# Optimization experiments

Hardware: AMD Instinct MI355X
Metric: run time of the kernel (lower is better)

The kernel has to match this reference:

```python
import jax, jax.numpy as jnp
import numpy as np

B, L_TEXT, N_TOKEN = 8, 2048, 2048
C_TEXT, C_OUT = 3584, 384
C_HID = C_OUT * 2
CHAIN_TYPES = (1, 2)   # heavy, light
CDR_TYPES = (2, 4, 6)  # CDR1/2/3


def setup_inputs() -> dict:
    key = jax.random.key(0)
    ks = jax.random.split(key, 10)
    text_conditioning = jax.random.normal(ks[0], (B, L_TEXT, C_TEXT), jnp.float32)
    text_mask = jnp.ones((B, L_TEXT), jnp.int32)
    chain_type_ids = jax.random.randint(ks[1], (B, L_TEXT), 0, 3).astype(jnp.int32)
    cdr_region_type_ids = jax.random.randint(ks[2], (B, L_TEXT), 0, 10).astype(jnp.int32)
    boltz_chain_type = jax.random.randint(ks[3], (B, N_TOKEN), 0, 4).astype(jnp.int32)
    boltz_region_type = jax.random.randint(ks[4], (B, N_TOKEN), 0, 10).astype(jnp.int32)
    W1 = jax.random.normal(ks[5], (C_HID, C_TEXT), jnp.float32) * 0.02
    b1 = jnp.zeros((C_HID,), jnp.float32)
    W2 = jax.random.normal(ks[6], (C_OUT, C_HID), jnp.float32) * 0.02
    b2 = jnp.zeros((C_OUT,), jnp.float32)
    scale = jnp.ones((1,), jnp.float32)
    return {
        "text_conditioning": text_conditioning, "text_mask": text_mask,
        "chain_type_ids": chain_type_ids, "cdr_region_type_ids": cdr_region_type_ids,
        "boltz_chain_type": boltz_chain_type, "boltz_region_type": boltz_region_type,
        "W1": W1, "b1": b1, "W2": W2, "b2": b2, "scale": scale,
    }


def _align_one(text_proj, tmask, pmask):
    # text_proj: [L, C]; tmask: [L] bool (text CDR positions); pmask: [N] bool (protein CDR positions)
    # The k-th masked text token (in sequence order) maps to the k-th masked protein token,
    # for k < min(n_text, n_protein). Other protein positions get zeros.
    L = tmask.shape[0]
    trank = jnp.cumsum(tmask) - 1          # rank among text CDR tokens
    n_text = jnp.sum(tmask)
    prank = jnp.cumsum(pmask) - 1          # rank among protein CDR tokens
    # idx_by_rank[r] = text index whose rank is r; out-of-range scatter indices dropped
    idx_by_rank = jnp.zeros((L,), jnp.int32).at[jnp.where(tmask, trank, L)].set(
        jnp.arange(L, dtype=jnp.int32), mode="drop")
    valid = pmask & (prank < n_text)       # prank < n_protein holds by construction under pmask
    src = idx_by_rank[jnp.clip(prank, 0, L - 1)]
    emb = text_proj[src]                   # [N, C]
    return jnp.where(valid[:, None], emb, jnp.zeros((), text_proj.dtype))


def reference(text_conditioning, text_mask, chain_type_ids, cdr_region_type_ids,
              boltz_chain_type, boltz_region_type, W1, b1, W2, b2, scale):
    # 2-layer MLP projection: c_text -> 2*c_out -> c_out with SiLU
    h = jax.nn.silu(jnp.einsum("blt,ht->blh", text_conditioning, W1) + b1)
    text_proj = jnp.einsum("blh,ch->blc", h, W2) + b2    # [B, L, C_OUT]

    tm = text_mask.astype(bool)
    result = jnp.zeros((text_conditioning.shape[0], boltz_chain_type.shape[1], W2.shape[0]),
                       text_proj.dtype)
    align = jax.vmap(_align_one)
    for ct in CHAIN_TYPES:
        for rt in CDR_TYPES:
            tmask = (chain_type_ids == ct) & (cdr_region_type_ids == rt) & tm
            pmask = (boltz_chain_type == ct) & (boltz_region_type == rt)
            # (chain, cdr) pairs write to disjoint protein positions, so add is exact
            result = result + align(text_proj, tmask, pmask)
    return scale * result
```

## Files before the change

kernel.cpp:

```cpp
#include <hip/hip_runtime.h>
#include <hip/hip_bf16.h>
#include <math.h>

typedef __bf16 bf16_t;
typedef bf16_t bf16x8 __attribute__((ext_vector_type(8)));
typedef bf16_t bf16x4 __attribute__((ext_vector_type(4)));
typedef float f32x4 __attribute__((ext_vector_type(4)));

#define L_TEXT 2048
#define N_TOKEN 2048
#define C_TEXT 3584
#define C_OUT 384
#define C_HID 768
#define BATCH 8
#define MAXROWS (BATCH * N_TOKEN)
#define PM 3072
#define KSPLIT 4
#define KCHUNK (C_TEXT / KSPLIT)
#define KSPLIT2 2
#define KCHUNK2 (C_HID / KSPLIT2)

__global__ __launch_bounds__(256) void cvt_kernel(const float* __restrict__ in,
                                                  bf16_t* __restrict__ out, int n) {
    int i = (blockIdx.x * 256 + threadIdx.x) * 8;
    if (i >= n) return;
    float4 v0 = *(const float4*)(in + i);
    float4 v1 = *(const float4*)(in + i + 4);
    bf16x8 o;
    o[0] = (bf16_t)v0.x; o[1] = (bf16_t)v0.y; o[2] = (bf16_t)v0.z; o[3] = (bf16_t)v0.w;
    o[4] = (bf16_t)v1.x; o[5] = (bf16_t)v1.y; o[6] = (bf16_t)v1.z; o[7] = (bf16_t)v1.w;
    *(bf16x8*)(out + i) = o;
}

__global__ void map_kernel(const int* __restrict__ tm, const int* __restrict__ ctid,
                           const int* __restrict__ cdrid, const int* __restrict__ bct,
                           const int* __restrict__ brt,
                           int* __restrict__ rows_src, int* __restrict__ inv,
                           int* __restrict__ count) {
    __shared__ int trow[L_TEXT];
    const int bp = blockIdx.x;
    const int b = bp / 6, p = bp % 6;
    const int ct = (p < 3) ? 1 : 2;
    const int rt = 2 + 2 * (p % 3);
    const int lane = threadIdx.x;
    const unsigned long long ltm = (1ull << lane) - 1ull;

    int base = 0;
    for (int l0 = 0; l0 < L_TEXT; l0 += 64) {
        int l = l0 + lane;
        bool m = (ctid[b * L_TEXT + l] == ct) && (cdrid[b * L_TEXT + l] == rt) &&
                 (tm[b * L_TEXT + l] != 0);
        unsigned long long bal = __ballot(m);
        if (m) trow[base + __popcll(bal & ltm)] = l;
        base += __popcll(bal);
    }
    const int n_text = base;
    __syncthreads();

    base = 0;
    for (int n0 = 0; n0 < N_TOKEN; n0 += 64) {
        int n = n0 + lane;
        bool pm = (bct[b * N_TOKEN + n] == ct) && (brt[b * N_TOKEN + n] == rt);
        unsigned long long bal = __ballot(pm);
        if (pm) {
            int pr = base + __popcll(bal & ltm);
            if (pr < n_text) {
                int i = atomicAdd(count, 1);
                if (i < PM) {
                    rows_src[i] = b * L_TEXT + trow[pr];
                    inv[b * N_TOKEN + n] = i;
                }
            }
        }
        base += __popcll(bal);
    }
}

__global__ __launch_bounds__(256) void gemm1_kernel(
    const float* __restrict__ X, const bf16_t* __restrict__ W1b,
    const int* __restrict__ rows_src, const int* __restrict__ countp,
    float* __restrict__ P) {
    const int count = *countp;
    const int m0 = blockIdx.x * 64;
    if (m0 >= count) return;
    const int n0 = blockIdx.y * 128;
    const int kbeg = blockIdx.z * KCHUNK;

    __shared__ __align__(16) bf16_t As[2][64][40];
    __shared__ __align__(16) bf16_t Bs[2][128][40];

    const int t = threadIdx.x;
    const int lane = t & 63;
    const int w = t >> 6;
    const int wr = w >> 1, wc = w & 1;
    const int fr = lane & 15;
    const int kq = (lane >> 4) * 8;

    f32x4 acc[2][4];
#pragma unroll
    for (int i = 0; i < 2; i++)
#pragma unroll
        for (int j = 0; j < 4; j++) acc[i][j] = (f32x4){0.f, 0.f, 0.f, 0.f};

    const int arow = t >> 2, ac8 = (t & 3) * 8;
    const bool av = (m0 + arow < count);
    const float* ap = X + (size_t)(av ? rows_src[m0 + arow] : 0) * C_TEXT + kbeg + ac8;
    const int aofs = arow * 40 + ac8;
    const bf16_t* bp[2];
    int bofs[2];
#pragma unroll
    for (int j = 0; j < 2; j++) {
        int c = t + 256 * j;
        int row = c >> 2, c8 = (c & 3) * 8;
        bp[j] = W1b + (size_t)(n0 + row) * C_TEXT + kbeg + c8;
        bofs[j] = row * 40 + c8;
    }

    bf16_t* AsF = &As[0][0][0];
    bf16_t* BsF = &Bs[0][0][0];
    const int ABUF = 64 * 40, BBUF = 128 * 40;

    bf16x8 ra, rb0, rb1;
    {
        float4 v0 = *(const float4*)(ap);
        float4 v1 = *(const float4*)(ap + 4);
        ra[0] = (bf16_t)v0.x; ra[1] = (bf16_t)v0.y; ra[2] = (bf16_t)v0.z; ra[3] = (bf16_t)v0.w;
        ra[4] = (bf16_t)v1.x; ra[5] = (bf16_t)v1.y; ra[6] = (bf16_t)v1.z; ra[7] = (bf16_t)v1.w;
        if (!av) { for (int e = 0; e < 8; e++) ra[e] = (bf16_t)0.0f; }
        rb0 = *(const bf16x8*)(bp[0]);
        rb1 = *(const bf16x8*)(bp[1]);
    }

    const int T = KCHUNK / 32;
    for (int tile = 0; tile < T; ++tile) {
        const int cur = tile & 1;
        *(bf16x8*)(AsF + cur * ABUF + aofs) = ra;
        *(bf16x8*)(BsF + cur * BBUF + bofs[0]) = rb0;
        *(bf16x8*)(BsF + cur * BBUF + bofs[1]) = rb1;
        if (tile + 1 < T) {
            int k = (tile + 1) * 32;
            float4 v0 = *(const float4*)(ap + k);
            float4 v1 = *(const float4*)(ap + k + 4);
            bf16x8 na;
            na[0] = (bf16_t)v0.x; na[1] = (bf16_t)v0.y; na[2] = (bf16_t)v0.z; na[3] = (bf16_t)v0.w;
            na[4] = (bf16_t)v1.x; na[5] = (bf16_t)v1.y; na[6] = (bf16_t)v1.z; na[7] = (bf16_t)v1.w;
            if (!av) { for (int e = 0; e < 8; e++) na[e] = (bf16_t)0.0f; }
            bf16x8 nb0 = *(const bf16x8*)(bp[0] + k);
            bf16x8 nb1 = *(const bf16x8*)(bp[1] + k);
            __syncthreads();
            bf16x8 af[2], bfr[4];
#pragma unroll
            for (int mi = 0; mi < 2; mi++)
                af[mi] = *(const bf16x8*)(AsF + cur * ABUF + (wr * 32 + mi * 16 + fr) * 40 + kq);
#pragma unroll
            for (int ni = 0; ni < 4; ni++)
                bfr[ni] = *(const bf16x8*)(BsF + cur * BBUF + (wc * 64 + ni * 16 + fr) * 40 + kq);
#pragma unroll
            for (int mi = 0; mi < 2; mi++)
#pragma unroll
                for (int ni = 0; ni < 4; ni++)
                    acc[mi][ni] = __builtin_amdgcn_mfma_f32_16x16x32_bf16(
                        af[mi], bfr[ni], acc[mi][ni], 0, 0, 0);
            ra = na; rb0 = nb0; rb1 = nb1;
        } else {
            __syncthreads();
            bf16x8 af[2], bfr[4];
#pragma unroll
            for (int mi = 0; mi < 2; mi++)
                af[mi] = *(const bf16x8*)(AsF + cur * ABUF + (wr * 32 + mi * 16 + fr) * 40 + kq);
#pragma unroll
            for (int ni = 0; ni < 4; ni++)
                bfr[ni] = *(const bf16x8*)(BsF + cur * BBUF + (wc * 64 + ni * 16 + fr) * 40 + kq);
#pragma unroll
            for (int mi = 0; mi < 2; mi++)
#pragma unroll
                for (int ni = 0; ni < 4; ni++)
                    acc[mi][ni] = __builtin_amdgcn_mfma_f32_16x16x32_bf16(
                        af[mi], bfr[ni], acc[mi][ni], 0, 0, 0);
        }
    }

    float* Pk = P + (size_t)blockIdx.z * PM * C_HID;
    const int rj = (lane >> 4) * 4;
#pragma unroll
    for (int mi = 0; mi < 2; mi++) {
#pragma unroll
        for (int ni = 0; ni < 4; ni++) {
            int gn = n0 + wc * 64 + ni * 16 + fr;
#pragma unroll
            for (int j = 0; j < 4; j++) {
                int gm = m0 + wr * 32 + mi * 16 + rj + j;
                if (gm < count) Pk[(size_t)gm * C_HID + gn] = acc[mi][ni][j];
            }
        }
    }
}

__global__ __launch_bounds__(256) void reduce1_kernel(
    const float* __restrict__ P, const float* __restrict__ b1,
    const int* __restrict__ countp, bf16_t* __restrict__ H) {
    const int count = *countp;
    int idx = blockIdx.x * 256 + threadIdx.x;
    int m = idx / (C_HID / 4);
    int c = (idx % (C_HID / 4)) * 4;
    if (m >= count) return;
    f32x4 s = *(const f32x4*)(P + (size_t)m * C_HID + c);
#pragma unroll
    for (int ks = 1; ks < KSPLIT; ks++)
        s += *(const f32x4*)(P + ((size_t)ks * PM + m) * C_HID + c);
    f32x4 bb = *(const f32x4*)(b1 + c);
    bf16x4 o;
#pragma unroll
    for (int j = 0; j < 4; j++) {
        float v = s[j] + bb[j];
        o[j] = (bf16_t)(v / (1.0f + __expf(-v)));
    }
    *(bf16x4*)(H + (size_t)m * C_HID + c) = o;
}

__global__ __launch_bounds__(256) void gemm2_kernel(
    const bf16_t* __restrict__ Hm, const bf16_t* __restrict__ W2b,
    const int* __restrict__ countp, float* __restrict__ P2) {
    const int count = *countp;
    const int m0 = blockIdx.x * 64;
    if (m0 >= count) return;
    const int n0 = blockIdx.y * 128;
    const int kbeg = blockIdx.z * KCHUNK2;

    __shared__ __align__(16) bf16_t As[2][64][40];
    __shared__ __align__(16) bf16_t Bs[2][128][40];

    const int t = threadIdx.x;
    const int lane = t & 63;
    const int w = t >> 6;
    const int wr = w >> 1, wc = w & 1;
    const int fr = lane & 15;
    const int kq = (lane >> 4) * 8;

    f32x4 acc[2][4];
#pragma unroll
    for (int i = 0; i < 2; i++)
#pragma unroll
        for (int j = 0; j < 4; j++) acc[i][j] = (f32x4){0.f, 0.f, 0.f, 0.f};

    const int arow = t >> 2, ac8 = (t & 3) * 8;
    const bf16_t* ap = Hm + (size_t)(m0 + arow) * C_HID + kbeg + ac8;
    const int aofs = arow * 40 + ac8;
    const bf16_t* bp[2];
    int bofs[2];
#pragma unroll
    for (int j = 0; j < 2; j++) {
        int c = t + 256 * j;
        int row = c >> 2, c8 = (c & 3) * 8;
        bp[j] = W2b + (size_t)(n0 + row) * C_HID + kbeg + c8;
        bofs[j] = row * 40 + c8;
    }

    bf16_t* AsF = &As[0][0][0];
    bf16_t* BsF = &Bs[0][0][0];
    const int ABUF = 64 * 40, BBUF = 128 * 40;

    bf16x8 ra = *(const bf16x8*)(ap);
    bf16x8 rb0 = *(const bf16x8*)(bp[0]);
    bf16x8 rb1 = *(const bf16x8*)(bp[1]);

    const int T = KCHUNK2 / 32;
    for (int tile = 0; tile < T; ++tile) {
        const int cur = tile & 1;
        *(bf16x8*)(AsF + cur * ABUF + aofs) = ra;
        *(bf16x8*)(BsF + cur * BBUF + bofs[0]) = rb0;
        *(bf16x8*)(BsF + cur * BBUF + bofs[1]) = rb1;
        bf16x8 na, nb0, nb1;
        bool more = (tile + 1 < T);
        if (more) {
            int k = (tile + 1) * 32;
            na = *(const bf16x8*)(ap + k);
            nb0 = *(const bf16x8*)(bp[0] + k);
            nb1 = *(const bf16x8*)(bp[1] + k);
        }
        __syncthreads();
        bf16x8 af[2], bfr[4];
#pragma unroll
        for (int mi = 0; mi < 2; mi++)
            af[mi] = *(const bf16x8*)(AsF + cur * ABUF + (wr * 32 + mi * 16 + fr) * 40 + kq);
#pragma unroll
        for (int ni = 0; ni < 4; ni++)
            bfr[ni] = *(const bf16x8*)(BsF + cur * BBUF + (wc * 64 + ni * 16 + fr) * 40 + kq);
#pragma unroll
        for (int mi = 0; mi < 2; mi++)
#pragma unroll
            for (int ni = 0; ni < 4; ni++)
                acc[mi][ni] = __builtin_amdgcn_mfma_f32_16x16x32_bf16(
                    af[mi], bfr[ni], acc[mi][ni], 0, 0, 0);
        if (more) { ra = na; rb0 = nb0; rb1 = nb1; }
    }

    float* Pk = P2 + (size_t)blockIdx.z * PM * C_OUT;
    const int rj = (lane >> 4) * 4;
#pragma unroll
    for (int mi = 0; mi < 2; mi++) {
#pragma unroll
        for (int ni = 0; ni < 4; ni++) {
            int gn = n0 + wc * 64 + ni * 16 + fr;
#pragma unroll
            for (int j = 0; j < 4; j++) {
                int gm = m0 + wr * 32 + mi * 16 + rj + j;
                if (gm < count) Pk[(size_t)gm * C_OUT + gn] = acc[mi][ni][j];
            }
        }
    }
}

__global__ __launch_bounds__(256) void out_kernel(
    const float* __restrict__ P2, const float* __restrict__ b2,
    const int* __restrict__ inv, const float* __restrict__ scale,
    float* __restrict__ out) {
    int idx = blockIdx.x * 256 + threadIdx.x;
    int token = idx / (C_OUT / 4);
    int c = (idx % (C_OUT / 4)) * 4;
    int m = inv[token];
    f32x4 o = (f32x4){0.f, 0.f, 0.f, 0.f};
    if (m >= 0) {
        f32x4 s = *(const f32x4*)(P2 + (size_t)m * C_OUT + c);
#pragma unroll
        for (int ks = 1; ks < KSPLIT2; ks++)
            s += *(const f32x4*)(P2 + ((size_t)ks * PM + m) * C_OUT + c);
        f32x4 bb = *(const f32x4*)(b2 + c);
        const float sc = scale[0];
#pragma unroll
        for (int j = 0; j < 4; j++) o[j] = sc * (s[j] + bb[j]);
    }
    *(f32x4*)(out + (size_t)token * C_OUT + c) = o;
}

extern "C" void kernel_launch(void* const* d_in, const int* in_sizes, int n_in,
                              void* d_out, int out_size, void* d_ws, size_t ws_size,
                              hipStream_t stream) {
    const float* X     = (const float*)d_in[0];
    const int*   tm    = (const int*)d_in[1];
    const int*   ctid  = (const int*)d_in[2];
    const int*   cdrid = (const int*)d_in[3];
    const int*   bct   = (const int*)d_in[4];
    const int*   brt   = (const int*)d_in[5];
    const float* W1    = (const float*)d_in[6];
    const float* b1    = (const float*)d_in[7];
    const float* W2    = (const float*)d_in[8];
    const float* b2    = (const float*)d_in[9];
    const float* scale = (const float*)d_in[10];

    char* ws = (char*)d_ws;
    size_t off = 0;
    int* count = (int*)(ws + off);        off += 1024;
    int* rows_src = (int*)(ws + off);     off += (size_t)PM * 4;
    int* inv = (int*)(ws + off);          off += (size_t)MAXROWS * 4;
    bf16_t* W1b = (bf16_t*)(ws + off);    off += (size_t)C_HID * C_TEXT * 2;
    bf16_t* W2b = (bf16_t*)(ws + off);    off += (size_t)C_OUT * C_HID * 2;
    bf16_t* H = (bf16_t*)(ws + off);      off += (size_t)PM * C_HID * 2;
    float* P = (float*)(ws + off);        off += (size_t)KSPLIT * PM * C_HID * 4;
    float* P2 = P;

    hipMemsetAsync(count, 0, 4, stream);
    hipMemsetAsync(inv, 0xFF, (size_t)MAXROWS * 4, stream);

    cvt_kernel<<<(C_HID * C_TEXT) / 2048, 256, 0, stream>>>(W1, W1b, C_HID * C_TEXT);
    cvt_kernel<<<(C_OUT * C_HID) / 2048, 256, 0, stream>>>(W2, W2b, C_OUT * C_HID);

    map_kernel<<<BATCH * 6, 64, 0, stream>>>(tm, ctid, cdrid, bct, brt,
                                             rows_src, inv, count);

    dim3 g1(PM / 64, C_HID / 128, KSPLIT);
    gemm1_kernel<<<g1, 256, 0, stream>>>(X, W1b, rows_src, count, P);

    reduce1_kernel<<<(PM * C_HID / 4) / 256, 256, 0, stream>>>(P, b1, count, H);

    dim3 g2(PM / 64, C_OUT / 128, KSPLIT2);
    gemm2_kernel<<<g2, 256, 0, stream>>>(H, W2b, count, P2);

    out_kernel<<<(MAXROWS * C_OUT / 4) / 256, 256, 0, stream>>>(
        P2, b2, inv, scale, (float*)d_out);
}
```

Baseline: 140.8 us.

## Fuse weight conversion and workspace init into one kernel; batch map_kernel loads

Two memsets and two bf16 conversion launches are merged into one kernel that converts W1 and W2, fills the inverse index with -1 and zeroes the counter. The map kernel now loads all mask inputs up front into per-lane bitmasks with unrolled loops, then runs the ballot/compaction passes from registers, so the global loads are no longer serialized with the ballots. This targets launch overhead and memory latency in the small setup stages at the cost of somewhat more register use.

```diff
diff --git a/kernel.cpp b/kernel.cpp
--- a/kernel.cpp
+++ b/kernel.cpp
@@ -20,23 +20,47 @@
 #define KSPLIT2 2
 #define KCHUNK2 (C_HID / KSPLIT2)
 
-__global__ __launch_bounds__(256) void cvt_kernel(const float* __restrict__ in,
-                                                  bf16_t* __restrict__ out, int n) {
-    int i = (blockIdx.x * 256 + threadIdx.x) * 8;
-    if (i >= n) return;
-    float4 v0 = *(const float4*)(in + i);
-    float4 v1 = *(const float4*)(in + i + 4);
-    bf16x8 o;
-    o[0] = (bf16_t)v0.x; o[1] = (bf16_t)v0.y; o[2] = (bf16_t)v0.z; o[3] = (bf16_t)v0.w;
-    o[4] = (bf16_t)v1.x; o[5] = (bf16_t)v1.y; o[6] = (bf16_t)v1.z; o[7] = (bf16_t)v1.w;
-    *(bf16x8*)(out + i) = o;
-}
-
-__global__ void map_kernel(const int* __restrict__ tm, const int* __restrict__ ctid,
-                           const int* __restrict__ cdrid, const int* __restrict__ bct,
-                           const int* __restrict__ brt,
-                           int* __restrict__ rows_src, int* __restrict__ inv,
-                           int* __restrict__ count) {
+#define NW1 (C_HID * C_TEXT / 8)
+#define NW2 (C_OUT * C_HID / 8)
+#define NINV (MAXROWS / 4)
+#define NINIT (NW1 + NW2 + NINV + 1)
+
+__global__ __launch_bounds__(256) void init_cvt_kernel(
+    const float* __restrict__ W1, const float* __restrict__ W2,
+    bf16_t* __restrict__ W1b, bf16_t* __restrict__ W2b,
+    int* __restrict__ inv, int* __restrict__ count) {
+    int idx = blockIdx.x * 256 + threadIdx.x;
+    if (idx < NW1) {
+        int i = idx * 8;
+        float4 v0 = *(const float4*)(W1 + i);
+        float4 v1 = *(const float4*)(W1 + i + 4);
+        bf16x8 o;
+        o[0] = (bf16_t)v0.x; o[1] = (bf16_t)v0.y; o[2] = (bf16_t)v0.z; o[3] = (bf16_t)v0.w;
+        o[4] = (bf16_t)v1.x; o[5] = (bf16_t)v1.y; o[6] = (bf16_t)v1.z; o[7] = (bf16_t)v1.w;
+        *(bf16x8*)(W1b + i) = o;
+    } else if (idx < NW1 + NW2) {
+        int i = (idx - NW1) * 8;
+        float4 v0 = *(const float4*)(W2 + i);
+        float4 v1 = *(const float4*)(W2 + i + 4);
+        bf16x8 o;
+        o[0] = (bf16_t)v0.x; o[1] = (bf16_t)v0.y; o[2] = (bf16_t)v0.z; o[3] = (bf16_t)v0.w;
+        o[4] = (bf16_t)v1.x; o[5] = (bf16_t)v1.y; o[6] = (bf16_t)v1.z; o[7] = (bf16_t)v1.w;
+        *(bf16x8*)(W2b + i) = o;
+    } else if (idx < NW1 + NW2 + NINV) {
+        int i = idx - NW1 - NW2;
+        int4 m1 = {-1, -1, -1, -1};
+        ((int4*)inv)[i] = m1;
+    } else if (idx == NW1 + NW2 + NINV) {
+        *count = 0;
+    }
+}
+
+__global__ __launch_bounds__(64) void map_kernel(
+    const int* __restrict__ tm, const int* __restrict__ ctid,
+    const int* __restrict__ cdrid, const int* __restrict__ bct,
+    const int* __restrict__ brt,
+    int* __restrict__ rows_src, int* __restrict__ inv,
+    int* __restrict__ count) {
     __shared__ int trow[L_TEXT];
     const int bp = blockIdx.x;
     const int b = bp / 6, p = bp % 6;
@@ -45,30 +69,46 @@
     const int lane = threadIdx.x;
     const unsigned long long ltm = (1ull << lane) - 1ull;
 
+    unsigned int tbits = 0, pbits = 0;
+#pragma unroll
+    for (int i = 0; i < 32; i++) {
+        int l = i * 64 + lane;
+        unsigned int m = (ctid[b * L_TEXT + l] == ct) &&
+                         (cdrid[b * L_TEXT + l] == rt) &&
+                         (tm[b * L_TEXT + l] != 0);
+        tbits |= m << i;
+    }
+#pragma unroll
+    for (int i = 0; i < 32; i++) {
+        int n = i * 64 + lane;
+        unsigned int m = (bct[b * N_TOKEN + n] == ct) &&
+                         (brt[b * N_TOKEN + n] == rt);
+        pbits |= m << i;
+    }
+
     int base = 0;
-    for (int l0 = 0; l0 < L_TEXT; l0 += 64) {
-        int l = l0 + lane;
-        bool m = (ctid[b * L_TEXT + l] == ct) && (cdrid[b * L_TEXT + l] == rt) &&
-                 (tm[b * L_TEXT + l] != 0);
+#pragma unroll
+    for (int i = 0; i < 32; i++) {
+        bool m = (tbits >> i) & 1;
         unsigned long long bal = __ballot(m);
-        if (m) trow[base + __popcll(bal & ltm)] = l;
+        if (m) trow[base + __popcll(bal & ltm)] = i * 64 + lane;
         base += __popcll(bal);
     }
     const int n_text = base;
     __syncthreads();
 
     base = 0;
-    for (int n0 = 0; n0 < N_TOKEN; n0 += 64) {
-        int n = n0 + lane;
-        bool pm = (bct[b * N_TOKEN + n] == ct) && (brt[b * N_TOKEN + n] == rt);
-        unsigned long long bal = __ballot(pm);
-        if (pm) {
+#pragma unroll
+    for (int i = 0; i < 32; i++) {
+        bool m = (pbits >> i) & 1;
+        unsigned long long bal = __ballot(m);
+        if (m) {
             int pr = base + __popcll(bal & ltm);
             if (pr < n_text) {
-                int i = atomicAdd(count, 1);
-                if (i < PM) {
-                    rows_src[i] = b * L_TEXT + trow[pr];
-                    inv[b * N_TOKEN + n] = i;
+                int idx = atomicAdd(count, 1);
+                if (idx < PM) {
+                    rows_src[idx] = b * L_TEXT + trow[pr];
+                    inv[b * N_TOKEN + i * 64 + lane] = idx;
                 }
             }
         }
@@ -359,11 +399,8 @@
     float* P = (float*)(ws + off);        off += (size_t)KSPLIT * PM * C_HID * 4;
     float* P2 = P;
 
-    hipMemsetAsync(count, 0, 4, stream);
-    hipMemsetAsync(inv, 0xFF, (size_t)MAXROWS * 4, stream);
-
-    cvt_kernel<<<(C_HID * C_TEXT) / 2048, 256, 0, stream>>>(W1, W1b, C_HID * C_TEXT);
-    cvt_kernel<<<(C_OUT * C_HID) / 2048, 256, 0, stream>>>(W2, W2b, C_OUT * C_HID);
+    init_cvt_kernel<<<(NINIT + 255) / 256, 256, 0, stream>>>(W1, W2, W1b, W2b,
+                                                             inv, count);
 
     map_kernel<<<BATCH * 6, 64, 0, stream>>>(tm, ctid, cdrid, bct, brt,
                                              rows_src, inv, count);
```

Measured after the change: 132.2 us. 6.1% less time.
